# Performance work log

Hardware: AMD Instinct MI355X
Metric: run time of the kernel (lower is better)

Reference implementation:

```python
import jax, jax.numpy as jnp
import numpy as np

EPS = 1e-4

def setup_inputs() -> dict:
    key = jax.random.key(0)
    x = jax.random.normal(key, (16, 256, 8192), dtype=jnp.float32)
    return {"x": x}

def reference(x):
    # x: [B, C, T]; cumulative (causal) normalization along time axis
    T = x.shape[-1]
    count = jnp.arange(1, T + 1, dtype=x.dtype).reshape(1, 1, T)
    cum_sum = jnp.cumsum(x, axis=-1)
    cum_pow_sum = jnp.cumsum(x * x, axis=-1)
    cum_mean = cum_sum / count
    cum_var = cum_pow_sum / count - cum_mean * cum_mean
    cum_std = jnp.sqrt(cum_var + EPS)
    return (x - cum_mean) / cum_std
```

## Files before the change

kernel.cpp:

```cpp
#include <hip/hip_runtime.h>

#define ROW_T   8192
#define THREADS 1024
#define ITEMS   8
#define NWAVES  (THREADS / 64)
#define EPSV    1e-4f

typedef float fvec4 __attribute__((ext_vector_type(4)));

__global__ __launch_bounds__(THREADS, 8)
void cumnorm_kernel(const float* __restrict__ x, float* __restrict__ out) {
    __shared__ float wbs[NWAVES];
    __shared__ float wbss[NWAVES];

    const int t    = threadIdx.x;
    const int lane = t & 63;
    const int wid  = t >> 6;

    const float* __restrict__ xr   = x   + (long long)blockIdx.x * ROW_T;
    float* __restrict__       outr = out + (long long)blockIdx.x * ROW_T;

    const int e0 = t * ITEMS;

    const fvec4 va = *reinterpret_cast<const fvec4*>(xr + e0);
    const fvec4 vb = *reinterpret_cast<const fvec4*>(xr + e0 + 4);

    float s  = ((va.x + va.y) + (va.z + va.w)) + ((vb.x + vb.y) + (vb.z + vb.w));
    float ss = fmaf(va.x, va.x, fmaf(va.y, va.y, fmaf(va.z, va.z, va.w * va.w)));
    ss = fmaf(vb.x, vb.x, fmaf(vb.y, vb.y, fmaf(vb.z, vb.z, fmaf(vb.w, vb.w, ss))));

    float is = s, iss = ss;
    #pragma unroll
    for (int off = 1; off < 64; off <<= 1) {
        const float us  = __shfl_up(is, off);
        const float uss = __shfl_up(iss, off);
        if (lane >= off) { is += us; iss += uss; }
    }
    if (lane == 63) { wbs[wid] = is; wbss[wid] = iss; }
    __syncthreads();

    float cs = 0.f, css = 0.f;
    #pragma unroll
    for (int w = 0; w < NWAVES; ++w) {
        const float a = wbs[w], b = wbss[w];
        if (w < wid) { cs += a; css += b; }
    }

    float S  = cs  + (is  - s);
    float SS = css + (iss - ss);

    fvec4 o0, o1;
#define CN_STEP(v, idx, dst) {                                            \
        S += (v); SS = fmaf((v), (v), SS);                                \
        const float inv  = __builtin_amdgcn_rcpf((float)(e0 + (idx) + 1));\
        const float mean = S * inv;                                       \
        const float var  = fmaf(SS, inv, -(mean * mean));                 \
        (dst) = ((v) - mean) * __builtin_amdgcn_rsqf(var + EPSV);         \
    }
    CN_STEP(va.x, 0, o0.x)
    CN_STEP(va.y, 1, o0.y)
    CN_STEP(va.z, 2, o0.z)
    CN_STEP(va.w, 3, o0.w)
    CN_STEP(vb.x, 4, o1.x)
    CN_STEP(vb.y, 5, o1.y)
    CN_STEP(vb.z, 6, o1.z)
    CN_STEP(vb.w, 7, o1.w)
#undef CN_STEP

    __builtin_nontemporal_store(o0, reinterpret_cast<fvec4*>(outr + e0));
    __builtin_nontemporal_store(o1, reinterpret_cast<fvec4*>(outr + e0 + 4));
}

extern "C" void kernel_launch(void* const* d_in, const int* in_sizes, int n_in,
                              void* d_out, int out_size, void* d_ws, size_t ws_size,
                              hipStream_t stream) {
    const float* x = (const float*)d_in[0];
    float* out = (float*)d_out;
    const int rows = out_size / ROW_T;
    cumnorm_kernel<<<rows, THREADS, 0, stream>>>(x, out);
}
```

Measured before the change: 236.6 us.

## Process multiple rows per block with register prefetch of next row

```diff
diff --git a/kernel.cpp b/kernel.cpp
--- a/kernel.cpp
+++ b/kernel.cpp
@@ -1,55 +1,76 @@
 #include <hip/hip_runtime.h>
 
 #define ROW_T   8192
-#define THREADS 1024
-#define ITEMS   8
+#define THREADS 512
+#define ITEMS   16
 #define NWAVES  (THREADS / 64)
+#define RPB     4
 #define EPSV    1e-4f
 
 typedef float fvec4 __attribute__((ext_vector_type(4)));
 
 __global__ __launch_bounds__(THREADS, 8)
 void cumnorm_kernel(const float* __restrict__ x, float* __restrict__ out) {
-    __shared__ float wbs[NWAVES];
-    __shared__ float wbss[NWAVES];
+    __shared__ float wbs[2][NWAVES];
+    __shared__ float wbss[2][NWAVES];
 
     const int t    = threadIdx.x;
     const int lane = t & 63;
     const int wid  = t >> 6;
 
-    const float* __restrict__ xr   = x   + (long long)blockIdx.x * ROW_T;
-    float* __restrict__       outr = out + (long long)blockIdx.x * ROW_T;
+    const float* __restrict__ xr   = x   + (long long)blockIdx.x * RPB * ROW_T;
+    float* __restrict__       outr = out + (long long)blockIdx.x * RPB * ROW_T;
 
     const int e0 = t * ITEMS;
 
-    const fvec4 va = *reinterpret_cast<const fvec4*>(xr + e0);
-    const fvec4 vb = *reinterpret_cast<const fvec4*>(xr + e0 + 4);
+    fvec4 c0 = *reinterpret_cast<const fvec4*>(xr + e0);
+    fvec4 c1 = *reinterpret_cast<const fvec4*>(xr + e0 + 4);
+    fvec4 c2 = *reinterpret_cast<const fvec4*>(xr + e0 + 8);
+    fvec4 c3 = *reinterpret_cast<const fvec4*>(xr + e0 + 12);
 
-    float s  = ((va.x + va.y) + (va.z + va.w)) + ((vb.x + vb.y) + (vb.z + vb.w));
-    float ss = fmaf(va.x, va.x, fmaf(va.y, va.y, fmaf(va.z, va.z, va.w * va.w)));
-    ss = fmaf(vb.x, vb.x, fmaf(vb.y, vb.y, fmaf(vb.z, vb.z, fmaf(vb.w, vb.w, ss))));
+    for (int r = 0; r < RPB; ++r) {
+        fvec4 n0, n1, n2, n3;
+        if (r + 1 < RPB) {
+            const float* nr = xr + (r + 1) * ROW_T + e0;
+            n0 = *reinterpret_cast<const fvec4*>(nr);
+            n1 = *reinterpret_cast<const fvec4*>(nr + 4);
+            n2 = *reinterpret_cast<const fvec4*>(nr + 8);
+            n3 = *reinterpret_cast<const fvec4*>(nr + 12);
+        }
 
-    float is = s, iss = ss;
-    #pragma unroll
-    for (int off = 1; off < 64; off <<= 1) {
-        const float us  = __shfl_up(is, off);
-        const float uss = __shfl_up(iss, off);
-        if (lane >= off) { is += us; iss += uss; }
-    }
-    if (lane == 63) { wbs[wid] = is; wbss[wid] = iss; }
-    __syncthreads();
+        float s = ((c0.x + c0.y) + (c0.z + c0.w)) + ((c1.x + c1.y) + (c1.z + c1.w))
+                + ((c2.x + c2.y) + (c2.z + c2.w)) + ((c3.x + c3.y) + (c3.z + c3.w));
+        float ss = fmaf(c0.x, c0.x, fmaf(c0.y, c0.y, fmaf(c0.z, c0.z, c0.w * c0.w)));
+        ss = fmaf(c1.x, c1.x, fmaf(c1.y, c1.y, fmaf(c1.z, c1.z, fmaf(c1.w, c1.w, ss))));
+        ss = fmaf(c2.x, c2.x, fmaf(c2.y, c2.y, fmaf(c2.z, c2.z, fmaf(c2.w, c2.w, ss))));
+        ss = fmaf(c3.x, c3.x, fmaf(c3.y, c3.y, fmaf(c3.z, c3.z, fmaf(c3.w, c3.w, ss))));
 
-    float cs = 0.f, css = 0.f;
-    #pragma unroll
-    for (int w = 0; w < NWAVES; ++w) {
-        const float a = wbs[w], b = wbss[w];
-        if (w < wid) { cs += a; css += b; }
-    }
+        float is = s, iss = ss;
+        #pragma unroll
+        for (int off = 1; off < 64; off <<= 1) {
+            const float us  = __shfl_up(is, off);
+            const float uss = __shfl_up(iss, off);
+            if (lane >= off) { is += us; iss += uss; }
+        }
+        if (lane == 63) { wbs[r & 1][wid] = is; wbss[r & 1][wid] = iss; }
+        __syncthreads();
 
-    float S  = cs  + (is  - s);
-    float SS = css + (iss - ss);
+        float a = wbs[r & 1][lane & (NWAVES - 1)];
+        float b = wbss[r & 1][lane & (NWAVES - 1)];
+        #pragma unroll
+        for (int off = 1; off < NWAVES; off <<= 1) {
+            const float ua = __shfl_up(a, off);
+            const float ub = __shfl_up(b, off);
+            if (lane >= off) { a += ua; b += ub; }
+        }
+        const float cs  = wid ? __shfl(a, wid - 1) : 0.f;
+        const float css = wid ? __shfl(b, wid - 1) : 0.f;
 
-    fvec4 o0, o1;
+        float S  = cs  + (is  - s);
+        float SS = css + (iss - ss);
+
+        float* __restrict__ orow = outr + (long long)r * ROW_T + e0;
+        fvec4 o;
 #define CN_STEP(v, idx, dst) {                                            \
         S += (v); SS = fmaf((v), (v), SS);                                \
         const float inv  = __builtin_amdgcn_rcpf((float)(e0 + (idx) + 1));\
@@ -57,18 +78,22 @@
         const float var  = fmaf(SS, inv, -(mean * mean));                 \
         (dst) = ((v) - mean) * __builtin_amdgcn_rsqf(var + EPSV);         \
     }
-    CN_STEP(va.x, 0, o0.x)
-    CN_STEP(va.y, 1, o0.y)
-    CN_STEP(va.z, 2, o0.z)
-    CN_STEP(va.w, 3, o0.w)
-    CN_STEP(vb.x, 4, o1.x)
-    CN_STEP(vb.y, 5, o1.y)
-    CN_STEP(vb.z, 6, o1.z)
-    CN_STEP(vb.w, 7, o1.w)
+        CN_STEP(c0.x,  0, o.x) CN_STEP(c0.y,  1, o.y)
+        CN_STEP(c0.z,  2, o.z) CN_STEP(c0.w,  3, o.w)
+        *reinterpret_cast<fvec4*>(orow) = o;
+        CN_STEP(c1.x,  4, o.x) CN_STEP(c1.y,  5, o.y)
+        CN_STEP(c1.z,  6, o.z) CN_STEP(c1.w,  7, o.w)
+        *reinterpret_cast<fvec4*>(orow + 4) = o;
+        CN_STEP(c2.x,  8, o.x) CN_STEP(c2.y,  9, o.y)
+        CN_STEP(c2.z, 10, o.z) CN_STEP(c2.w, 11, o.w)
+        *reinterpret_cast<fvec4*>(orow + 8) = o;
+        CN_STEP(c3.x, 12, o.x) CN_STEP(c3.y, 13, o.y)
+        CN_STEP(c3.z, 14, o.z) CN_STEP(c3.w, 15, o.w)
+        *reinterpret_cast<fvec4*>(orow + 12) = o;
 #undef CN_STEP
 
-    __builtin_nontemporal_store(o0, reinterpret_cast<fvec4*>(outr + e0));
-    __builtin_nontemporal_store(o1, reinterpret_cast<fvec4*>(outr + e0 + 4));
+        if (r + 1 < RPB) { c0 = n0; c1 = n1; c2 = n2; c3 = n3; }
+    }
 }
 
 extern "C" void kernel_launch(void* const* d_in, const int* in_sizes, int n_in,
@@ -77,5 +102,5 @@
     const float* x = (const float*)d_in[0];
     float* out = (float*)d_out;
     const int rows = out_size / ROW_T;
-    cumnorm_kernel<<<rows, THREADS, 0, stream>>>(x, out);
+    cumnorm_kernel<<<rows / RPB, THREADS, 0, stream>>>(x, out);
 }
```

Result: slower. 263.6 us (+11.4%).

## Process each row with one wave using DPP scans and a chunked carry pipeline

Applied to the files above, without the earlier changes.

```diff
diff --git a/kernel.cpp b/kernel.cpp
--- a/kernel.cpp
+++ b/kernel.cpp
@@ -1,55 +1,67 @@
 #include <hip/hip_runtime.h>
 
 #define ROW_T   8192
-#define THREADS 1024
-#define ITEMS   8
-#define NWAVES  (THREADS / 64)
+#define THREADS 256
+#define WPB     4
+#define NT      32
+#define PIPE    8
 #define EPSV    1e-4f
 
 typedef float fvec4 __attribute__((ext_vector_type(4)));
 
-__global__ __launch_bounds__(THREADS, 8)
+template<int CTRL, int RM>
+__device__ __forceinline__ float dpp_add(float v) {
+    const int p = __builtin_amdgcn_update_dpp(0, __float_as_int(v), CTRL, RM, 0xf, true);
+    return v + __int_as_float(p);
+}
+
+__device__ __forceinline__ float wave_incl_scan(float v) {
+    v = dpp_add<0x111, 0xf>(v);
+    v = dpp_add<0x112, 0xf>(v);
+    v = dpp_add<0x114, 0xf>(v);
+    v = dpp_add<0x118, 0xf>(v);
+    v = dpp_add<0x142, 0xa>(v);
+    v = dpp_add<0x143, 0xc>(v);
+    return v;
+}
+
+__global__ __launch_bounds__(THREADS, 4)
 void cumnorm_kernel(const float* __restrict__ x, float* __restrict__ out) {
-    __shared__ float wbs[NWAVES];
-    __shared__ float wbss[NWAVES];
+    const int lane = threadIdx.x & 63;
+    const int wid  = threadIdx.x >> 6;
 
-    const int t    = threadIdx.x;
-    const int lane = t & 63;
-    const int wid  = t >> 6;
+    const long long row = (long long)blockIdx.x * WPB + wid;
+    const float* __restrict__ xr   = x   + row * ROW_T;
+    float* __restrict__       outr = out + row * ROW_T;
+    const int l4 = lane * 4;
 
-    const float* __restrict__ xr   = x   + (long long)blockIdx.x * ROW_T;
-    float* __restrict__       outr = out + (long long)blockIdx.x * ROW_T;
+    fvec4 B[PIPE];
+    #pragma unroll
+    for (int k = 0; k < PIPE; ++k)
+        B[k] = *reinterpret_cast<const fvec4*>(xr + k * 256 + l4);
 
-    const int e0 = t * ITEMS;
+    float carry_s = 0.f, carry_ss = 0.f;
 
-    const fvec4 va = *reinterpret_cast<const fvec4*>(xr + e0);
-    const fvec4 vb = *reinterpret_cast<const fvec4*>(xr + e0 + 4);
+    #pragma unroll
+    for (int k = 0; k < NT; ++k) {
+        const fvec4 c = B[k & (PIPE - 1)];
+        if (k + PIPE < NT)
+            B[k & (PIPE - 1)] = *reinterpret_cast<const fvec4*>(xr + (k + PIPE) * 256 + l4);
 
-    float s  = ((va.x + va.y) + (va.z + va.w)) + ((vb.x + vb.y) + (vb.z + vb.w));
-    float ss = fmaf(va.x, va.x, fmaf(va.y, va.y, fmaf(va.z, va.z, va.w * va.w)));
-    ss = fmaf(vb.x, vb.x, fmaf(vb.y, vb.y, fmaf(vb.z, vb.z, fmaf(vb.w, vb.w, ss))));
+        float s  = (c.x + c.y) + (c.z + c.w);
+        float ss = fmaf(c.x, c.x, fmaf(c.y, c.y, fmaf(c.z, c.z, c.w * c.w)));
 
-    float is = s, iss = ss;
-    #pragma unroll
-    for (int off = 1; off < 64; off <<= 1) {
-        const float us  = __shfl_up(is, off);
-        const float uss = __shfl_up(iss, off);
-        if (lane >= off) { is += us; iss += uss; }
-    }
-    if (lane == 63) { wbs[wid] = is; wbss[wid] = iss; }
-    __syncthreads();
+        const float is  = wave_incl_scan(s);
+        const float iss = wave_incl_scan(ss);
 
-    float cs = 0.f, css = 0.f;
-    #pragma unroll
-    for (int w = 0; w < NWAVES; ++w) {
-        const float a = wbs[w], b = wbss[w];
-        if (w < wid) { cs += a; css += b; }
-    }
+        float S  = carry_s  + (is  - s);
+        float SS = carry_ss + (iss - ss);
 
-    float S  = cs  + (is  - s);
-    float SS = css + (iss - ss);
+        carry_s  += __int_as_float(__builtin_amdgcn_readlane(__float_as_int(is),  63));
+        carry_ss += __int_as_float(__builtin_amdgcn_readlane(__float_as_int(iss), 63));
 
-    fvec4 o0, o1;
+        const int e0 = k * 256 + l4;
+        fvec4 o;
 #define CN_STEP(v, idx, dst) {                                            \
         S += (v); SS = fmaf((v), (v), SS);                                \
         const float inv  = __builtin_amdgcn_rcpf((float)(e0 + (idx) + 1));\
@@ -57,18 +69,14 @@
         const float var  = fmaf(SS, inv, -(mean * mean));                 \
         (dst) = ((v) - mean) * __builtin_amdgcn_rsqf(var + EPSV);         \
     }
-    CN_STEP(va.x, 0, o0.x)
-    CN_STEP(va.y, 1, o0.y)
-    CN_STEP(va.z, 2, o0.z)
-    CN_STEP(va.w, 3, o0.w)
-    CN_STEP(vb.x, 4, o1.x)
-    CN_STEP(vb.y, 5, o1.y)
-    CN_STEP(vb.z, 6, o1.z)
-    CN_STEP(vb.w, 7, o1.w)
+        CN_STEP(c.x, 0, o.x)
+        CN_STEP(c.y, 1, o.y)
+        CN_STEP(c.z, 2, o.z)
+        CN_STEP(c.w, 3, o.w)
 #undef CN_STEP
 
-    __builtin_nontemporal_store(o0, reinterpret_cast<fvec4*>(outr + e0));
-    __builtin_nontemporal_store(o1, reinterpret_cast<fvec4*>(outr + e0 + 4));
+        *reinterpret_cast<fvec4*>(outr + e0) = o;
+    }
 }
 
 extern "C" void kernel_launch(void* const* d_in, const int* in_sizes, int n_in,
@@ -77,5 +85,5 @@
     const float* x = (const float*)d_in[0];
     float* out = (float*)d_out;
     const int rows = out_size / ROW_T;
-    cumnorm_kernel<<<rows, THREADS, 0, stream>>>(x, out);
+    cumnorm_kernel<<<rows / WPB, THREADS, 0, stream>>>(x, out);
 }
```

Result: no change. 232.9 us (-1.5%).
